# Optimization experiments

Hardware: AMD Instinct MI355X
Metric: run time of the kernel (lower is better)

## Reference

```python
import jax, jax.numpy as jnp
import numpy as np

N_NODES = 20000
N_RELS = 64
RP = 8
EMB = 64
N_CLASSES = 16
NT = 250000      # unique (subject, object) pairs
N_TRIPLES = 500000


def setup_inputs() -> dict:
    rng = np.random.default_rng(0)
    # sample candidate (s, o) pairs, dedupe (mirrors torch.unique(pairs, dim=0)),
    # keep exactly NT unique pairs
    cand = rng.integers(0, N_NODES, size=(NT + 60000, 2))
    pairs = np.unique(cand, axis=0)
    assert pairs.shape[0] >= NT
    pairs = pairs[:NT]
    # each triple maps to a unique-pair row and a relation column;
    # relation_matrix is the coalesced sparse_coo (nt, num_rels) densified
    row = rng.integers(0, NT, size=N_TRIPLES)
    rel = rng.integers(0, N_RELS, size=N_TRIPLES)
    relation_matrix = np.zeros((NT, N_RELS), dtype=np.float32)
    np.add.at(relation_matrix, (row, rel), 1.0)
    # hindices / vindices exactly as in __init__ (note the literal o*r / s*r):
    s, o = pairs[:, 0].astype(np.int64), pairs[:, 1].astype(np.int64)
    rm = np.arange(RP, dtype=np.int64)[:, None]
    hrow = np.tile(s, RP)                      # (RP*NT,) row in [0, N)
    hcol = (o[None, :] * rm).reshape(-1)       # (RP*NT,) col in [0, N*RP)
    vrow = (s[None, :] * rm).reshape(-1)       # (RP*NT,) row in [0, N*RP)
    vcol = np.tile(o, RP)                      # (RP*NT,) col in [0, N)

    key = jax.random.key(0)
    ks = jax.random.split(key, 6)

    def xavier(k, shape, fan_in, fan_out):
        gain = np.float32(np.sqrt(2.0))  # calculate_gain('relu')
        bound = gain * np.float32(np.sqrt(6.0 / (fan_in + fan_out)))
        return jax.random.uniform(k, shape, jnp.float32, -bound, bound)

    lb = np.float32(1.0 / np.sqrt(N_RELS))  # nn.Linear default init bound
    return {
        "relation_matrix": jnp.asarray(relation_matrix),
        "hrow": jnp.asarray(hrow), "hcol": jnp.asarray(hcol),
        "vrow": jnp.asarray(vrow), "vcol": jnp.asarray(vcol),
        "W_l1": jax.random.uniform(ks[0], (N_RELS, RP), jnp.float32, -lb, lb),
        "b_l1": jax.random.uniform(ks[1], (RP,), jnp.float32, -lb, lb),
        "W_l2": jax.random.uniform(ks[2], (N_RELS, RP), jnp.float32, -lb, lb),
        "b_l2": jax.random.uniform(ks[3], (RP,), jnp.float32, -lb, lb),
        "weights1": xavier(ks[4], (RP, N_NODES, EMB), N_NODES * EMB, RP * EMB),
        "weights2": xavier(ks[5], (RP, EMB, N_CLASSES), EMB * N_CLASSES, RP * N_CLASSES),
        "bias1": jnp.zeros((EMB,), jnp.float32),
        "bias2": jnp.zeros((N_CLASSES,), jnp.float32),
    }


def reference(relation_matrix, hrow, hcol, vrow, vcol,
              W_l1, b_l1, W_l2, b_l2, weights1, weights2, bias1, bias2):
    n, rp, e = N_NODES, RP, EMB
    nrp = n * rp
    # ---- hop 1: latent coefficients (to_latent1, ldepth=0 => single Linear)
    l1 = relation_matrix @ W_l1 + b_l1              # (NT, RP)
    l1 = l1.T.reshape(-1)                           # (RP*NT,) r-major, matches h/v index order
    # sum_sparse(hindices, l1, (n, n*rp), row=False): per-edge column-sum normalization
    colsum = jax.ops.segment_sum(l1, hcol, num_segments=nrp)
    l1 = l1 / colsum[hcol]
    # spmm over hindices: out[hrow] += l1 * weights1.view(n*rp, e)[hcol]
    Wflat = weights1.reshape(nrp, e)                # (N*RP, EMB)
    h = jax.ops.segment_sum(l1[:, None] * Wflat[hcol], hrow, num_segments=n)
    h = jax.nn.relu(h + bias1)                      # (N, EMB)
    # ---- hop 2
    l2 = jax.nn.softmax(relation_matrix @ W_l2 + b_l2, axis=1)  # (NT, RP)
    l2 = jax.nn.relu(l2.T.reshape(-1))              # (RP*NT,)
    # sum_sparse(vindices, l2, (n*rp, n), row=True): per-edge row-sum normalization
    rowsum = jax.ops.segment_sum(l2, vrow, num_segments=nrp)
    l2 = l2 / jnp.maximum(rowsum[vrow], 1e-6)
    # spmm over vindices: out[vrow] += l2 * h[vcol]
    h2 = jax.ops.segment_sum(l2[:, None] * h[vcol], vrow, num_segments=nrp)
    h2 = h2.reshape(rp, n, e)                       # (RP, N, EMB)
    logits = jnp.einsum('rhc,rnh->nc', weights2, h2) + bias2  # (N, C)
    return logits
```

## Files before the change

### kernel.cpp

```cpp
#include <hip/hip_runtime.h>
#include <hip/hip_fp16.h>

#define NT      250000
#define NN      20000
#define RP      8
#define EMB     64
#define NCLS    16
#define NRELS   64
#define COLB    547
#define REDB    64
#define KMAX    140000

__global__ __launch_bounds__(256) void k_gemv(
    const float* __restrict__ rm,
    const float* __restrict__ W1, const float* __restrict__ b1,
    const float* __restrict__ W2, const float* __restrict__ b2,
    float* __restrict__ l1, float* __restrict__ l2)
{
    __shared__ float tile[256 * 20];
    int t = threadIdx.x;
    int base = blockIdx.x * 256;
    float a1[8], a2[8];
#pragma unroll
    for (int r = 0; r < 8; ++r) { a1[r] = b1[r]; a2[r] = b2[r]; }

#pragma unroll 1
    for (int kc = 0; kc < 4; ++kc) {
        __syncthreads();
#pragma unroll
        for (int q = 0; q < 4; ++q) {
            int i = q * 256 + t;
            int pl = i >> 2, j4 = i & 3;
            int p = base + pl;
            float4 v = make_float4(0.f, 0.f, 0.f, 0.f);
            if (p < NT) v = reinterpret_cast<const float4*>(rm)[(size_t)p * 16 + kc * 4 + j4];
            *reinterpret_cast<float4*>(&tile[pl * 20 + j4 * 4]) = v;
        }
        __syncthreads();
        float xr[16];
#pragma unroll
        for (int j4 = 0; j4 < 4; ++j4) {
            float4 v = *reinterpret_cast<const float4*>(&tile[t * 20 + j4 * 4]);
            xr[j4 * 4 + 0] = v.x; xr[j4 * 4 + 1] = v.y;
            xr[j4 * 4 + 2] = v.z; xr[j4 * 4 + 3] = v.w;
        }
#pragma unroll
        for (int kk = 0; kk < 16; ++kk) {
            float x = xr[kk];
            int k = kc * 16 + kk;
#pragma unroll
            for (int r = 0; r < 8; ++r) {
                a1[r] = fmaf(x, W1[k * 8 + r], a1[r]);
                a2[r] = fmaf(x, W2[k * 8 + r], a2[r]);
            }
        }
    }
    int p = base + t;
    if (p >= NT) return;
    float mx = a2[0];
#pragma unroll
    for (int r = 1; r < 8; ++r) mx = fmaxf(mx, a2[r]);
    float sm = 0.f;
#pragma unroll
    for (int r = 0; r < 8; ++r) { a2[r] = __expf(a2[r] - mx); sm += a2[r]; }
    float inv = 1.0f / sm;
#pragma unroll
    for (int r = 0; r < 8; ++r) a2[r] *= inv;
    float4* o1 = reinterpret_cast<float4*>(l1 + (size_t)p * 8);
    float4* o2 = reinterpret_cast<float4*>(l2 + (size_t)p * 8);
    o1[0] = make_float4(a1[0], a1[1], a1[2], a1[3]);
    o1[1] = make_float4(a1[4], a1[5], a1[6], a1[7]);
    o2[0] = make_float4(a2[0], a2[1], a2[2], a2[3]);
    o2[1] = make_float4(a2[4], a2[5], a2[6], a2[7]);
}

__global__ __launch_bounds__(256) void k_rowptr(
    const int* __restrict__ hrow, int* __restrict__ rowptr)
{
    int i = blockIdx.x * blockDim.x + threadIdx.x;
    if (i > NN) return;
    int lo = 0, hi = NT;
    while (lo < hi) { int mid = (lo + hi) >> 1; if (hrow[mid] < i) lo = mid + 1; else hi = mid; }
    rowptr[i] = lo;
}

__global__ __launch_bounds__(256) void k_hist(
    const int* __restrict__ vcol, int* __restrict__ cnt)
{
    int p = blockIdx.x * blockDim.x + threadIdx.x;
    if (p < NT) atomicAdd(&cnt[vcol[p]], 1);
}

__global__ __launch_bounds__(1024) void k_scan(
    const int* __restrict__ cnt, int* __restrict__ cstart, int* __restrict__ cnt2)
{
    __shared__ int part[1024];
    int t = threadIdx.x;
    int base = t * 20;
    int local[20];
    int s = 0;
#pragma unroll
    for (int i = 0; i < 20; ++i) {
        int idx = base + i;
        int c = (idx < NN) ? cnt[idx] : 0;
        local[i] = s;
        s += c;
    }
    part[t] = s;
    __syncthreads();
    for (int off = 1; off < 1024; off <<= 1) {
        int v = (t >= off) ? part[t - off] : 0;
        __syncthreads();
        part[t] += v;
        __syncthreads();
    }
    int ebase = t ? part[t - 1] : 0;
#pragma unroll
    for (int i = 0; i < 20; ++i) {
        int idx = base + i;
        if (idx < NN) { cstart[idx] = ebase + local[i]; cnt2[idx] = ebase + local[i]; }
    }
    if (t == 1023) cstart[NN] = part[1023];
}

__global__ __launch_bounds__(256) void k_pos(
    const int* __restrict__ vcol, int* __restrict__ cnt2, int* __restrict__ cscidx)
{
    int p = blockIdx.x * blockDim.x + threadIdx.x;
    if (p >= NT) return;
    int o = vcol[p];
    int slot = atomicAdd(&cnt2[o], 1);
    cscidx[slot] = p;
}

__global__ __launch_bounds__(256) void k_colsum(
    const float* __restrict__ l1, const int* __restrict__ cstart,
    const int* __restrict__ cscidx, float* __restrict__ colsum)
{
    int bid = blockIdx.x;
    if (bid < COLB) {
        int tid = bid * 256 + threadIdx.x;
        if (tid < NN * 7) {
            int o = tid / 7;
            int r = tid - o * 7 + 1;
            int qb = cstart[o], qe = cstart[o + 1];
            float s = 0.f;
            for (int q = qb; q < qe; ++q)
                s += l1[(size_t)cscidx[q] * 8 + r];
            atomicAdd(&colsum[o * r], s);
        }
    } else {
        int b2 = bid - COLB;
        float s = 0.f;
        for (int i = b2 * 256 + threadIdx.x; i < NT; i += REDB * 256) s += l1[(size_t)i * 8];
        __shared__ float red[256];
        red[threadIdx.x] = s;
        __syncthreads();
        for (int off = 128; off > 0; off >>= 1) {
            if (threadIdx.x < off) red[threadIdx.x] += red[threadIdx.x + off];
            __syncthreads();
        }
        if (threadIdx.x == 0) atomicAdd(&colsum[0], red[0]);
    }
}

__global__ __launch_bounds__(256) void k_inv(float* __restrict__ cs)
{
    int i = blockIdx.x * blockDim.x + threadIdx.x;
    if (i < RP * NN) cs[i] = 1.0f / cs[i];
}

__global__ __launch_bounds__(256) void k_contrib(
    const float* __restrict__ l1, const float* __restrict__ ics,
    const int* __restrict__ cstart, const int* __restrict__ cscidx,
    const float* __restrict__ w1, __half* __restrict__ contrib)
{
    int o = (int)((blockIdx.x * blockDim.x + threadIdx.x) >> 6);
    int lane = threadIdx.x & 63;
    if (o >= NN) return;
    int qb = cstart[o], qe = cstart[o + 1];
    if (qb == qe) return;
    float y[8];
    y[0] = w1[lane] * ics[0];
#pragma unroll
    for (int r = 1; r < 8; ++r) {
        int seg = o * r;
        y[r] = w1[(size_t)seg * EMB + lane] * ics[seg];
    }
    for (int q = qb; q < qe; ++q) {
        int p = cscidx[q];
        const float4* lp4 = reinterpret_cast<const float4*>(l1 + (size_t)p * 8);
        float4 A = lp4[0], B = lp4[1];
        float v = A.x * y[0];
        v = fmaf(A.y, y[1], v); v = fmaf(A.z, y[2], v); v = fmaf(A.w, y[3], v);
        v = fmaf(B.x, y[4], v); v = fmaf(B.y, y[5], v);
        v = fmaf(B.z, y[6], v); v = fmaf(B.w, y[7], v);
        contrib[(size_t)p * EMB + lane] = __float2half(v);
    }
}

__global__ __launch_bounds__(256) void k_h(
    const __half* __restrict__ contrib, const float* __restrict__ l2,
    const int* __restrict__ rowptr, const float* __restrict__ bias1,
    __half* __restrict__ h, float* __restrict__ rowsum, float* __restrict__ rs0part)
{
    int s = (int)((blockIdx.x * blockDim.x + threadIdx.x) >> 6);
    int lane = threadIdx.x & 63;
    if (s >= NN) return;
    int pb = rowptr[s], pe = rowptr[s + 1];
    float acc = 0.f;
    for (int p = pb; p < pe; ++p)
        acc += __half2float(contrib[(size_t)p * EMB + lane]);
    h[(size_t)s * EMB + lane] = __float2half(fmaxf(acc + bias1[lane], 0.f));

    float psum = 0.f;
    for (int p0 = pb + (lane >> 3); p0 < pe; p0 += 8)
        psum += l2[(size_t)p0 * 8 + (lane & 7)];
    psum += __shfl_xor(psum, 8, 64);
    psum += __shfl_xor(psum, 16, 64);
    psum += __shfl_xor(psum, 32, 64);
    if (s == 0) {
        float tt = psum;
        tt += __shfl_xor(tt, 1, 64);
        tt += __shfl_xor(tt, 2, 64);
        tt += __shfl_xor(tt, 4, 64);
        if (lane == 0) rs0part[0] = tt;
    } else {
        if (lane == 0) rs0part[s] = psum;
        else if (lane < 8) atomicAdd(&rowsum[s * lane], psum);
    }
}

__global__ __launch_bounds__(256) void k_redrs(
    const float* __restrict__ rs0part, float* __restrict__ rowsum)
{
    __shared__ float red[256];
    float sv = 0.f;
    for (int i = threadIdx.x; i < NN; i += 256) sv += rs0part[i];
    red[threadIdx.x] = sv;
    __syncthreads();
    for (int off = 128; off > 0; off >>= 1) {
        if (threadIdx.x < off) red[threadIdx.x] += red[threadIdx.x + off];
        __syncthreads();
    }
    if (threadIdx.x == 0) rowsum[0] = 1.0f / fmaxf(red[0], 1e-6f);
}

__global__ __launch_bounds__(256) void k_misc(
    float* __restrict__ rs, float* __restrict__ out, const float* __restrict__ b2)
{
    int i = blockIdx.x * blockDim.x + threadIdx.x;
    if (i >= 1 && i < KMAX) rs[i] = 1.0f / fmaxf(rs[i], 1e-6f);
    if (i < NN * NCLS) out[i] = b2[i & (NCLS - 1)];
}

__global__ __launch_bounds__(256) void k_l2out(
    const float* __restrict__ l2, const int* __restrict__ rowptr,
    const int* __restrict__ vcol, const __half* __restrict__ h,
    const float* __restrict__ irs, const float* __restrict__ w2,
    float* __restrict__ out, float* __restrict__ Abuf0)
{
    __shared__ float lacc[4][8 * 64];
    int w = threadIdx.x >> 6;
    int lane = threadIdx.x & 63;
    int g = w >> 1, sub = w & 1;
    int s = blockIdx.x * 2 + g;
    int pb = rowptr[s], pe = rowptr[s + 1];
    float sc[8];
#pragma unroll
    for (int rr = 1; rr < 8; ++rr) sc[rr] = (s > 0) ? irs[s * rr] : 0.f;
    float acc[8];
#pragma unroll
    for (int r = 0; r < 8; ++r) acc[r] = 0.f;
    int half = (pe - pb + 1) >> 1;
    int mb = pb + sub * half;
    int me = sub ? pe : pb + half;
    int p = mb;
    for (; p + 3 < me; p += 4) {
        int o0 = vcol[p], o1 = vcol[p + 1], o2 = vcol[p + 2], o3 = vcol[p + 3];
        float hv0 = __half2float(h[(size_t)o0 * EMB + lane]);
        float hv1 = __half2float(h[(size_t)o1 * EMB + lane]);
        float hv2 = __half2float(h[(size_t)o2 * EMB + lane]);
        float hv3 = __half2float(h[(size_t)o3 * EMB + lane]);
        const float4* q4 = reinterpret_cast<const float4*>(l2 + (size_t)p * 8);
        float4 A = q4[0], B = q4[1], C = q4[2], D = q4[3];
        float4 E = q4[4], F = q4[5], G = q4[6], H = q4[7];
        acc[0] = fmaf(A.x, hv0, fmaf(C.x, hv1, fmaf(E.x, hv2, fmaf(G.x, hv3, acc[0]))));
        acc[1] = fmaf(A.y, hv0, fmaf(C.y, hv1, fmaf(E.y, hv2, fmaf(G.y, hv3, acc[1]))));
        acc[2] = fmaf(A.z, hv0, fmaf(C.z, hv1, fmaf(E.z, hv2, fmaf(G.z, hv3, acc[2]))));
        acc[3] = fmaf(A.w, hv0, fmaf(C.w, hv1, fmaf(E.w, hv2, fmaf(G.w, hv3, acc[3]))));
        acc[4] = fmaf(B.x, hv0, fmaf(D.x, hv1, fmaf(F.x, hv2, fmaf(H.x, hv3, acc[4]))));
        acc[5] = fmaf(B.y, hv0, fmaf(D.y, hv1, fmaf(F.y, hv2, fmaf(H.y, hv3, acc[5]))));
        acc[6] = fmaf(B.z, hv0, fmaf(D.z, hv1, fmaf(F.z, hv2, fmaf(H.z, hv3, acc[6]))));
        acc[7] = fmaf(B.w, hv0, fmaf(D.w, hv1, fmaf(F.w, hv2, fmaf(H.w, hv3, acc[7]))));
    }
    for (; p < me; ++p) {
        int o0 = vcol[p];
        float hv0 = __half2float(h[(size_t)o0 * EMB + lane]);
        const float4* q4 = reinterpret_cast<const float4*>(l2 + (size_t)p * 8);
        float4 A = q4[0], B = q4[1];
        acc[0] = fmaf(A.x, hv0, acc[0]); acc[1] = fmaf(A.y, hv0, acc[1]);
        acc[2] = fmaf(A.z, hv0, acc[2]); acc[3] = fmaf(A.w, hv0, acc[3]);
        acc[4] = fmaf(B.x, hv0, acc[4]); acc[5] = fmaf(B.y, hv0, acc[5]);
        acc[6] = fmaf(B.z, hv0, acc[6]); acc[7] = fmaf(B.w, hv0, acc[7]);
    }
#pragma unroll
    for (int r = 0; r < 8; ++r) lacc[w][r * 64 + lane] = acc[r];
    __syncthreads();
    float ca[8];
#pragma unroll
    for (int r = 0; r < 8; ++r)
        ca[r] = lacc[2 * g][r * 64 + lane] + lacc[2 * g + 1][r * 64 + lane];
    if (s == 0) {
        if (sub == 0) {
            float a = ca[0] + ca[1] + ca[2] + ca[3] + ca[4] + ca[5] + ca[6] + ca[7];
            Abuf0[lane] = a;
        }
        return;
    }
    if (sub == 0) Abuf0[(size_t)s * EMB + lane] = ca[0];
    if (pb == pe) return;
    int hq = lane >> 4, c = lane & 15;
    int rlo = sub ? 4 : 1, rhi = sub ? 8 : 4;
    for (int rr = rlo; rr < rhi; ++rr) {
        int k = s * rr;
        int rp = k / NN;
        int n  = k - rp * NN;
        float a = ca[rr];
        float v = 0.f;
#pragma unroll
        for (int hh = 0; hh < 16; ++hh) {
            float av = __shfl(a, hq * 16 + hh, 64);
            v = fmaf(av, w2[((rp * EMB) + (hq * 16 + hh)) * NCLS + c], v);
        }
        v += __shfl_xor(v, 16, 64);
        v += __shfl_xor(v, 32, 64);
        if (lane < 16) atomicAdd(&out[(size_t)n * NCLS + lane], v * sc[rr]);
    }
}

__global__ __launch_bounds__(256) void k_redA(
    const float* __restrict__ Abuf0, float* __restrict__ h0row)
{
    __shared__ float red[256];
    int lane = threadIdx.x & 63, w = threadIdx.x >> 6;
    float sum = 0.f;
    for (int ss = blockIdx.x + 64 * w; ss < NN; ss += 256)
        sum += Abuf0[(size_t)ss * EMB + lane];
    red[threadIdx.x] = sum;
    __syncthreads();
    if (threadIdx.x < 64) {
        float v = red[threadIdx.x] + red[threadIdx.x + 64] +
                  red[threadIdx.x + 128] + red[threadIdx.x + 192];
        atomicAdd(&h0row[threadIdx.x], v);
    }
}

__global__ __launch_bounds__(64) void k_out0(
    const float* __restrict__ h0row, const float* __restrict__ irs0,
    const float* __restrict__ w2, float* __restrict__ out)
{
    int hq = threadIdx.x >> 4, c = threadIdx.x & 15;
    float v = 0.f;
#pragma unroll
    for (int hh = 0; hh < 16; ++hh) {
        int hd = hq * 16 + hh;
        v = fmaf(h0row[hd], w2[hd * NCLS + c], v);
    }
    v += __shfl_xor(v, 16, 64);
    v += __shfl_xor(v, 32, 64);
    if (threadIdx.x < 16) atomicAdd(&out[c], v * irs0[0]);
}

extern "C" void kernel_launch(void* const* d_in, const int* in_sizes, int n_in,
                              void* d_out, int out_size, void* d_ws, size_t ws_size,
                              hipStream_t stream)
{
    const float* rm    = (const float*)d_in[0];
    const int*   hrow  = (const int*)d_in[1];
    const int*   vcol  = (const int*)d_in[4];
    const float* W1    = (const float*)d_in[5];
    const float* b1    = (const float*)d_in[6];
    const float* W2    = (const float*)d_in[7];
    const float* b2    = (const float*)d_in[8];
    const float* w1    = (const float*)d_in[9];
    const float* w2    = (const float*)d_in[10];
    const float* bias1 = (const float*)d_in[11];
    const float* bias2 = (const float*)d_in[12];
    float* out = (float*)d_out;

    float* ws = (float*)d_ws;
    float*  l1      = ws;
    float*  l2      = ws + 2000000;
    int*    rowptr  = (int*)(ws + 4000000);
    float*  h0row   = ws + 4030000;
    float*  colsum  = ws + 4100000;
    float*  rowsum  = ws + 4260000;
    __half* h       = (__half*)(ws + 4400000);
    int*    cnt     = (int*)(ws + 5040000);
    int*    cstart  = cnt + 20000;
    int*    cnt2    = cstart + 20001;
    int*    cscidx  = cnt2 + 20000;
    __half* contrib = (__half*)(ws + 5600000);
    float*  Abuf0   = ws;
    float*  rs0part = ws + 1280000;

    hipMemsetAsync(colsum, 0, (size_t)160000 * sizeof(float), stream);
    hipMemsetAsync(rowsum, 0, (size_t)KMAX * sizeof(float), stream);
    hipMemsetAsync(h0row, 0, (size_t)64 * sizeof(float), stream);
    hipMemsetAsync(cnt, 0, (size_t)20000 * sizeof(int), stream);

    k_rowptr <<<(NN + 256) / 256, 256, 0, stream>>>(hrow, rowptr);
    k_hist   <<<(NT + 255) / 256, 256, 0, stream>>>(vcol, cnt);
    k_scan   <<<1, 1024, 0, stream>>>(cnt, cstart, cnt2);
    k_pos    <<<(NT + 255) / 256, 256, 0, stream>>>(vcol, cnt2, cscidx);
    k_gemv   <<<(NT + 255) / 256, 256, 0, stream>>>(rm, W1, b1, W2, b2, l1, l2);
    k_colsum <<<COLB + REDB, 256, 0, stream>>>(l1, cstart, cscidx, colsum);
    k_inv    <<<(RP * NN + 255) / 256, 256, 0, stream>>>(colsum);
    k_contrib<<<(NN * 64) / 256, 256, 0, stream>>>(l1, colsum, cstart, cscidx, w1, contrib);
    k_h      <<<(NN * 64) / 256, 256, 0, stream>>>(contrib, l2, rowptr, bias1, h, rowsum, rs0part);
    k_redrs  <<<1, 256, 0, stream>>>(rs0part, rowsum);
    k_misc   <<<(NN * NCLS + 255) / 256, 256, 0, stream>>>(rowsum, out, bias2);
    k_l2out  <<<NN / 2, 256, 0, stream>>>(l2, rowptr, vcol, h, rowsum, w2, out, Abuf0);
    k_redA   <<<64, 256, 0, stream>>>(Abuf0, h0row);
    k_out0   <<<1, 64, 0, stream>>>(h0row, rowsum, w2, out);
}
```

Measured before the change: 264.9 us.

## Merge small kernels and simplify l2out to one wave per row

Folds the rowptr binary search and the vcol histogram into a single launch, and folds the rowsum[0] reduction into k_misc as an extra block, cutting two kernel launches. The contrib loop is unrolled by two so more independent loads are in flight. k_l2out drops its two-wave split with LDS merging and __syncthreads, and now gives each source row to one wave that handles all seven relation projections. This removes the shared-memory traffic and barrier but halves the parallelism per row, which may leave latency exposed on rows with many edges.

Result: faster. 251.3 us (-5.1%).

```diff
diff --git a/kernel.cpp b/kernel.cpp
--- a/kernel.cpp
+++ b/kernel.cpp
@@ -10,6 +10,9 @@
 #define COLB    547
 #define REDB    64
 #define KMAX    140000
+#define RPB     79
+#define HIB     977
+#define MISCB   1250
 
 __global__ __launch_bounds__(256) void k_gemv(
     const float* __restrict__ rm,
@@ -74,21 +77,21 @@
     o2[1] = make_float4(a2[4], a2[5], a2[6], a2[7]);
 }
 
-__global__ __launch_bounds__(256) void k_rowptr(
-    const int* __restrict__ hrow, int* __restrict__ rowptr)
-{
-    int i = blockIdx.x * blockDim.x + threadIdx.x;
-    if (i > NN) return;
-    int lo = 0, hi = NT;
-    while (lo < hi) { int mid = (lo + hi) >> 1; if (hrow[mid] < i) lo = mid + 1; else hi = mid; }
-    rowptr[i] = lo;
-}
-
-__global__ __launch_bounds__(256) void k_hist(
+__global__ __launch_bounds__(256) void k_init(
+    const int* __restrict__ hrow, int* __restrict__ rowptr,
     const int* __restrict__ vcol, int* __restrict__ cnt)
 {
-    int p = blockIdx.x * blockDim.x + threadIdx.x;
-    if (p < NT) atomicAdd(&cnt[vcol[p]], 1);
+    int bid = blockIdx.x;
+    if (bid < RPB) {
+        int i = bid * 256 + threadIdx.x;
+        if (i > NN) return;
+        int lo = 0, hi = NT;
+        while (lo < hi) { int mid = (lo + hi) >> 1; if (hrow[mid] < i) lo = mid + 1; else hi = mid; }
+        rowptr[i] = lo;
+    } else {
+        int p = (bid - RPB) * 256 + threadIdx.x;
+        if (p < NT) atomicAdd(&cnt[vcol[p]], 1);
+    }
 }
 
 __global__ __launch_bounds__(1024) void k_scan(
@@ -187,15 +190,32 @@
         int seg = o * r;
         y[r] = w1[(size_t)seg * EMB + lane] * ics[seg];
     }
-    for (int q = qb; q < qe; ++q) {
-        int p = cscidx[q];
-        const float4* lp4 = reinterpret_cast<const float4*>(l1 + (size_t)p * 8);
-        float4 A = lp4[0], B = lp4[1];
-        float v = A.x * y[0];
-        v = fmaf(A.y, y[1], v); v = fmaf(A.z, y[2], v); v = fmaf(A.w, y[3], v);
-        v = fmaf(B.x, y[4], v); v = fmaf(B.y, y[5], v);
-        v = fmaf(B.z, y[6], v); v = fmaf(B.w, y[7], v);
-        contrib[(size_t)p * EMB + lane] = __float2half(v);
+    int q = qb;
+    for (; q + 1 < qe; q += 2) {
+        int p0 = cscidx[q], p1 = cscidx[q + 1];
+        const float4* a4 = reinterpret_cast<const float4*>(l1 + (size_t)p0 * 8);
+        const float4* b4 = reinterpret_cast<const float4*>(l1 + (size_t)p1 * 8);
+        float4 A = a4[0], B = a4[1], C = b4[0], D = b4[1];
+        float v0 = A.x * y[0];
+        v0 = fmaf(A.y, y[1], v0); v0 = fmaf(A.z, y[2], v0); v0 = fmaf(A.w, y[3], v0);
+        v0 = fmaf(B.x, y[4], v0); v0 = fmaf(B.y, y[5], v0);
+        v0 = fmaf(B.z, y[6], v0); v0 = fmaf(B.w, y[7], v0);
+        float v1 = C.x * y[0];
+        v1 = fmaf(C.y, y[1], v1); v1 = fmaf(C.z, y[2], v1); v1 = fmaf(C.w, y[3], v1);
+        v1 = fmaf(D.x, y[4], v1); v1 = fmaf(D.y, y[5], v1);
+        v1 = fmaf(D.z, y[6], v1); v1 = fmaf(D.w, y[7], v1);
+        contrib[(size_t)p0 * EMB + lane] = __float2half(v0);
+        contrib[(size_t)p1 * EMB + lane] = __float2half(v1);
+    }
+    if (q < qe) {
+        int p0 = cscidx[q];
+        const float4* a4 = reinterpret_cast<const float4*>(l1 + (size_t)p0 * 8);
+        float4 A = a4[0], B = a4[1];
+        float v0 = A.x * y[0];
+        v0 = fmaf(A.y, y[1], v0); v0 = fmaf(A.z, y[2], v0); v0 = fmaf(A.w, y[3], v0);
+        v0 = fmaf(B.x, y[4], v0); v0 = fmaf(B.y, y[5], v0);
+        v0 = fmaf(B.z, y[6], v0); v0 = fmaf(B.w, y[7], v0);
+        contrib[(size_t)p0 * EMB + lane] = __float2half(v0);
     }
 }
 
@@ -231,27 +251,27 @@
     }
 }
 
-__global__ __launch_bounds__(256) void k_redrs(
-    const float* __restrict__ rs0part, float* __restrict__ rowsum)
-{
-    __shared__ float red[256];
-    float sv = 0.f;
-    for (int i = threadIdx.x; i < NN; i += 256) sv += rs0part[i];
-    red[threadIdx.x] = sv;
-    __syncthreads();
-    for (int off = 128; off > 0; off >>= 1) {
-        if (threadIdx.x < off) red[threadIdx.x] += red[threadIdx.x + off];
-        __syncthreads();
-    }
-    if (threadIdx.x == 0) rowsum[0] = 1.0f / fmaxf(red[0], 1e-6f);
-}
-
 __global__ __launch_bounds__(256) void k_misc(
-    float* __restrict__ rs, float* __restrict__ out, const float* __restrict__ b2)
-{
-    int i = blockIdx.x * blockDim.x + threadIdx.x;
-    if (i >= 1 && i < KMAX) rs[i] = 1.0f / fmaxf(rs[i], 1e-6f);
-    if (i < NN * NCLS) out[i] = b2[i & (NCLS - 1)];
+    float* __restrict__ rs, float* __restrict__ out, const float* __restrict__ b2,
+    const float* __restrict__ rs0part)
+{
+    int bid = blockIdx.x;
+    if (bid < MISCB) {
+        int i = bid * 256 + threadIdx.x;
+        if (i >= 1 && i < KMAX) rs[i] = 1.0f / fmaxf(rs[i], 1e-6f);
+        if (i < NN * NCLS) out[i] = b2[i & (NCLS - 1)];
+    } else {
+        __shared__ float red[256];
+        float sv = 0.f;
+        for (int i = threadIdx.x; i < NN; i += 256) sv += rs0part[i];
+        red[threadIdx.x] = sv;
+        __syncthreads();
+        for (int off = 128; off > 0; off >>= 1) {
+            if (threadIdx.x < off) red[threadIdx.x] += red[threadIdx.x + off];
+            __syncthreads();
+        }
+        if (threadIdx.x == 0) rs[0] = 1.0f / fmaxf(red[0], 1e-6f);
+    }
 }
 
 __global__ __launch_bounds__(256) void k_l2out(
@@ -260,11 +280,9 @@
     const float* __restrict__ irs, const float* __restrict__ w2,
     float* __restrict__ out, float* __restrict__ Abuf0)
 {
-    __shared__ float lacc[4][8 * 64];
-    int w = threadIdx.x >> 6;
+    int s = (int)((blockIdx.x * blockDim.x + threadIdx.x) >> 6);
     int lane = threadIdx.x & 63;
-    int g = w >> 1, sub = w & 1;
-    int s = blockIdx.x * 2 + g;
+    if (s >= NN) return;
     int pb = rowptr[s], pe = rowptr[s + 1];
     float sc[8];
 #pragma unroll
@@ -272,11 +290,8 @@
     float acc[8];
 #pragma unroll
     for (int r = 0; r < 8; ++r) acc[r] = 0.f;
-    int half = (pe - pb + 1) >> 1;
-    int mb = pb + sub * half;
-    int me = sub ? pe : pb + half;
-    int p = mb;
-    for (; p + 3 < me; p += 4) {
+    int p = pb;
+    for (; p + 3 < pe; p += 4) {
         int o0 = vcol[p], o1 = vcol[p + 1], o2 = vcol[p + 2], o3 = vcol[p + 3];
         float hv0 = __half2float(h[(size_t)o0 * EMB + lane]);
         float hv1 = __half2float(h[(size_t)o1 * EMB + lane]);
@@ -294,7 +309,7 @@
         acc[6] = fmaf(B.z, hv0, fmaf(D.z, hv1, fmaf(F.z, hv2, fmaf(H.z, hv3, acc[6]))));
         acc[7] = fmaf(B.w, hv0, fmaf(D.w, hv1, fmaf(F.w, hv2, fmaf(H.w, hv3, acc[7]))));
     }
-    for (; p < me; ++p) {
+    for (; p < pe; ++p) {
         int o0 = vcol[p];
         float hv0 = __half2float(h[(size_t)o0 * EMB + lane]);
         const float4* q4 = reinterpret_cast<const float4*>(l2 + (size_t)p * 8);
@@ -304,33 +319,24 @@
         acc[4] = fmaf(B.x, hv0, acc[4]); acc[5] = fmaf(B.y, hv0, acc[5]);
         acc[6] = fmaf(B.z, hv0, acc[6]); acc[7] = fmaf(B.w, hv0, acc[7]);
     }
-#pragma unroll
-    for (int r = 0; r < 8; ++r) lacc[w][r * 64 + lane] = acc[r];
-    __syncthreads();
-    float ca[8];
-#pragma unroll
-    for (int r = 0; r < 8; ++r)
-        ca[r] = lacc[2 * g][r * 64 + lane] + lacc[2 * g + 1][r * 64 + lane];
     if (s == 0) {
-        if (sub == 0) {
-            float a = ca[0] + ca[1] + ca[2] + ca[3] + ca[4] + ca[5] + ca[6] + ca[7];
-            Abuf0[lane] = a;
-        }
+        float a = acc[0] + acc[1] + acc[2] + acc[3] +
+                  acc[4] + acc[5] + acc[6] + acc[7];
+        Abuf0[lane] = a;
         return;
     }
-    if (sub == 0) Abuf0[(size_t)s * EMB + lane] = ca[0];
+    Abuf0[(size_t)s * EMB + lane] = acc[0];
     if (pb == pe) return;
     int hq = lane >> 4, c = lane & 15;
-    int rlo = sub ? 4 : 1, rhi = sub ? 8 : 4;
-    for (int rr = rlo; rr < rhi; ++rr) {
+#pragma unroll
+    for (int rr = 1; rr < 8; ++rr) {
         int k = s * rr;
         int rp = k / NN;
         int n  = k - rp * NN;
-        float a = ca[rr];
         float v = 0.f;
 #pragma unroll
         for (int hh = 0; hh < 16; ++hh) {
-            float av = __shfl(a, hq * 16 + hh, 64);
+            float av = __shfl(acc[rr], hq * 16 + hh, 64);
             v = fmaf(av, w2[((rp * EMB) + (hq * 16 + hh)) * NCLS + c], v);
         }
         v += __shfl_xor(v, 16, 64);
@@ -410,8 +416,7 @@
     hipMemsetAsync(h0row, 0, (size_t)64 * sizeof(float), stream);
     hipMemsetAsync(cnt, 0, (size_t)20000 * sizeof(int), stream);
 
-    k_rowptr <<<(NN + 256) / 256, 256, 0, stream>>>(hrow, rowptr);
-    k_hist   <<<(NT + 255) / 256, 256, 0, stream>>>(vcol, cnt);
+    k_init   <<<RPB + HIB, 256, 0, stream>>>(hrow, rowptr, vcol, cnt);
     k_scan   <<<1, 1024, 0, stream>>>(cnt, cstart, cnt2);
     k_pos    <<<(NT + 255) / 256, 256, 0, stream>>>(vcol, cnt2, cscidx);
     k_gemv   <<<(NT + 255) / 256, 256, 0, stream>>>(rm, W1, b1, W2, b2, l1, l2);
@@ -419,9 +424,8 @@
     k_inv    <<<(RP * NN + 255) / 256, 256, 0, stream>>>(colsum);
     k_contrib<<<(NN * 64) / 256, 256, 0, stream>>>(l1, colsum, cstart, cscidx, w1, contrib);
     k_h      <<<(NN * 64) / 256, 256, 0, stream>>>(contrib, l2, rowptr, bias1, h, rowsum, rs0part);
-    k_redrs  <<<1, 256, 0, stream>>>(rs0part, rowsum);
-    k_misc   <<<(NN * NCLS + 255) / 256, 256, 0, stream>>>(rowsum, out, bias2);
-    k_l2out  <<<NN / 2, 256, 0, stream>>>(l2, rowptr, vcol, h, rowsum, w2, out, Abuf0);
+    k_misc   <<<MISCB + 1, 256, 0, stream>>>(rowsum, out, bias2, rs0part);
+    k_l2out  <<<(NN * 64) / 256, 256, 0, stream>>>(l2, rowptr, vcol, h, rowsum, w2, out, Abuf0);
     k_redA   <<<64, 256, 0, stream>>>(Abuf0, h0row);
     k_out0   <<<1, 64, 0, stream>>>(h0row, rowsum, w2, out);
 }
```
